# Kernel tuning notes

Measured on AMD Instinct MI355X. Metric: run time of the kernel, lower is better.

Reference implementation:

```python
import jax, jax.numpy as jnp
import numpy as np

N_EMBD = 1024
N_HEAD = 16
HEAD_DIM = N_EMBD // N_HEAD


def setup_inputs() -> dict:
    key = jax.random.key(0)
    ks = jax.random.split(key, 9)
    s = 1.0 / np.sqrt(N_EMBD)
    x = jax.random.normal(ks[0], (2, 2048, N_EMBD), dtype=jnp.float32)
    # PyTorch Linear weights stored as (out_features, in_features)
    Wq = jax.random.uniform(ks[1], (N_EMBD, N_EMBD), jnp.float32, -s, s)
    bq = jax.random.uniform(ks[2], (N_EMBD,), jnp.float32, -s, s)
    Wk = jax.random.uniform(ks[3], (N_EMBD, N_EMBD), jnp.float32, -s, s)
    bk = jax.random.uniform(ks[4], (N_EMBD,), jnp.float32, -s, s)
    Wv = jax.random.uniform(ks[5], (N_EMBD, N_EMBD), jnp.float32, -s, s)
    bv = jax.random.uniform(ks[6], (N_EMBD,), jnp.float32, -s, s)
    Wfc = jax.random.uniform(ks[7], (N_EMBD, N_EMBD), jnp.float32, -s, s)
    bfc = jax.random.uniform(ks[8], (N_EMBD,), jnp.float32, -s, s)
    return {"x": x, "Wq": Wq, "bq": bq, "Wk": Wk, "bk": bk,
            "Wv": Wv, "bv": bv, "Wfc": Wfc, "bfc": bfc}


def reference(x, Wq, bq, Wk, bk, Wv, bv, Wfc, bfc):
    B, S, _ = x.shape

    def proj(W, b):
        y = jnp.einsum('bsd,ed->bse', x, W) + b  # Linear: x @ W.T + b
        return y.reshape(B, S, N_HEAD, HEAD_DIM).transpose(0, 2, 1, 3)  # [B,H,S,Dh]

    q = proj(Wq, bq)
    k = proj(Wk, bk)
    v = proj(Wv, bv)
    scores = jnp.einsum('bhqd,bhkd->bhqk', q, k) / jnp.sqrt(jnp.float32(HEAD_DIM))
    weights = jax.nn.softmax(scores, axis=-1)  # [B,H,S,S]
    out = jnp.einsum('bhqk,bhkd->bhqd', weights, v)
    out = out.transpose(0, 2, 1, 3).reshape(B, S, N_EMBD)
    out = jnp.einsum('bsd,ed->bse', out, Wfc) + bfc
    return (out, weights)
```

## Files before the change

### kernel.cpp

```cpp
#include <hip/hip_runtime.h>
#include <hip/hip_bf16.h>
#include <stdint.h>


typedef __attribute__((ext_vector_type(8))) short bf16x8;
typedef __attribute__((ext_vector_type(4))) short bf16x4;
typedef __attribute__((ext_vector_type(4))) float f32x4;

#define MFMA16(a, b, c) __builtin_amdgcn_mfma_f32_16x16x32_bf16(a, b, c, 0, 0, 0)
#define EXP2(x) __builtin_amdgcn_exp2f(x)

__device__ __forceinline__ short f2bf(float x) {
  uint32_t u = __builtin_bit_cast(uint32_t, x);
  u += 0x7FFFu + ((u >> 16) & 1u);
  return (short)(u >> 16);
}

__device__ __forceinline__ uint32_t cvtpk_bf16(float lo, float hi) {
  uint32_t r;
  asm("v_cvt_pk_bf16_f32 %0, %1, %2" : "=v"(r) : "v"(lo), "v"(hi));
  return r;
}

__device__ __forceinline__ void gload16(const void* g, void* l) {
  __builtin_amdgcn_global_load_lds((const __attribute__((address_space(1))) uint32_t*)g,
                                   (__attribute__((address_space(3))) uint32_t*)l, 16, 0, 0);
}

__global__ __launch_bounds__(256) void cvt_k(const float* __restrict__ src,
                                             short* __restrict__ dst, int n4) {
  int i = blockIdx.x * 256 + threadIdx.x;
  if (i < n4) {
    f32x4 v = *(const f32x4*)(src + (size_t)i * 4);
    bf16x4 o;
    o[0] = f2bf(v[0]); o[1] = f2bf(v[1]); o[2] = f2bf(v[2]); o[3] = f2bf(v[3]);
    *(bf16x4*)(dst + (size_t)i * 4) = o;
  }
}

__global__ __launch_bounds__(256) void cvtw_k(
    const float* __restrict__ w0, const float* __restrict__ w1,
    const float* __restrict__ w2, const float* __restrict__ w3,
    short* __restrict__ dst) {
  const int which = blockIdx.x >> 10;
  const float* src = which == 0 ? w0 : which == 1 ? w1 : which == 2 ? w2 : w3;
  const int i = (blockIdx.x & 1023) * 256 + threadIdx.x;
  f32x4 v = *(const f32x4*)(src + (size_t)i * 4);
  bf16x4 o;
  o[0] = f2bf(v[0]); o[1] = f2bf(v[1]); o[2] = f2bf(v[2]); o[3] = f2bf(v[3]);
  *(bf16x4*)(dst + (size_t)which * 1048576 + (size_t)i * 4) = o;
}

template <int EPI>
__global__ __launch_bounds__(256) void gemm_k(
    const short* __restrict__ A, const short* __restrict__ B,
    const float* __restrict__ bq, const float* __restrict__ bk,
    const float* __restrict__ bv,
    short* __restrict__ Qb, short* __restrict__ Kb, short* __restrict__ Vt,
    float* __restrict__ Fout) {
  const int K = 1024;
  __shared__ short sA[128 * 32];
  __shared__ short sB[128 * 32];
  const int tid = threadIdx.x;
  const int w = tid >> 6, lane = tid & 63;
  const int wr = w >> 1, wc = w & 1;
  const int lrow = lane & 15, lk = (lane >> 4) * 8;
  const int tileM = blockIdx.x * 128, tileN = blockIdx.y * 128;

  f32x4 acc[4][4];
#pragma unroll
  for (int i = 0; i < 4; ++i)
#pragma unroll
    for (int j = 0; j < 4; ++j) acc[i][j] = (f32x4){0.f, 0.f, 0.f, 0.f};

  for (int k0 = 0; k0 < K; k0 += 32) {
#pragma unroll
    for (int i = 0; i < 2; ++i) {
      int u = (w * 2 + i) * 64 + lane;
      int row = u >> 2, c8 = (u & 3) * 8;
      gload16(A + (size_t)(tileM + row) * K + k0 + c8, (short*)sA + (w * 2 + i) * 512);
      gload16(B + (size_t)(tileN + row) * K + k0 + c8, (short*)sB + (w * 2 + i) * 512);
    }
    __syncthreads();
    bf16x8 af[4], bfr[4];
#pragma unroll
    for (int mi = 0; mi < 4; ++mi)
      af[mi] = *(const bf16x8*)&sA[(wr * 64 + mi * 16 + lrow) * 32 + lk];
#pragma unroll
    for (int ni = 0; ni < 4; ++ni)
      bfr[ni] = *(const bf16x8*)&sB[(wc * 64 + ni * 16 + lrow) * 32 + lk];
#pragma unroll
    for (int mi = 0; mi < 4; ++mi)
#pragma unroll
      for (int ni = 0; ni < 4; ++ni)
        acc[mi][ni] = MFMA16(af[mi], bfr[ni], acc[mi][ni]);
    __syncthreads();
  }

#pragma unroll
  for (int mi = 0; mi < 4; ++mi) {
    int m0 = tileM + wr * 64 + mi * 16 + (lane >> 4) * 4;
#pragma unroll
    for (int ni = 0; ni < 4; ++ni) {
      int n = tileN + wc * 64 + ni * 16 + lrow;
      f32x4 v = acc[mi][ni];
      if (EPI == 0) {
        int which = n >> 10, e = n & 1023;
        int h = e >> 6, dh = e & 63;
        float bias = (which == 0 ? bq : which == 1 ? bk : bv)[e];
        int b = m0 >> 11, s0 = m0 & 2047;
        size_t hb = (size_t)(b * 16 + h);
        if (which == 2) {
          int kt2 = s0 >> 5, gl = (s0 >> 3) & 3, ni2 = dh >> 4, j = dh & 15;
          size_t base = (((hb * 64 + kt2) * 4 + ni2) * 64 + gl * 16 + j) * 8 + (s0 & 7);
          bf16x4 pk;
#pragma unroll
          for (int r = 0; r < 4; ++r) pk[r] = f2bf(v[r] + bias);
          *(bf16x4*)&Vt[base] = pk;
        } else {
          short* dst = (which == 0) ? Qb : Kb;
          int tile = s0 >> 4, h2 = dh >> 5, gl = (dh >> 3) & 3, ci = dh & 7;
          size_t base = (((hb * 128 + tile) * 2 + h2) * 64 + gl * 16 + (s0 & 15)) * 8 + ci;
#pragma unroll
          for (int r = 0; r < 4; ++r) dst[base + r * 8] = f2bf(v[r] + bias);
        }
      } else {
        float bias = bq[n];
#pragma unroll
        for (int r = 0; r < 4; ++r)
          Fout[(size_t)(m0 + r) * 1024 + n] = v[r] + bias;
      }
    }
  }
}

__device__ __forceinline__ void sw1_phase(bf16x8& pa, bf16x8& pb, int nxt,
    const short* __restrict__ Kf, int l8, const bf16x8& aQ0, const bf16x8& aQ1,
    float kscale, float& ls0, float& ls1, float& ls2, float& ls3) {
  const f32x4 zero = {0.f, 0.f, 0.f, 0.f};
  __builtin_amdgcn_s_setprio(1);
  f32x4 s = MFMA16(pa, aQ0, zero);
  s = MFMA16(pb, aQ1, s);
  __builtin_amdgcn_s_setprio(0);
  pa = *(const bf16x8*)&Kf[nxt * 1024 + l8];
  pb = *(const bf16x8*)&Kf[nxt * 1024 + 512 + l8];
  ls0 += EXP2(s[0] * kscale);
  ls1 += EXP2(s[1] * kscale);
  ls2 += EXP2(s[2] * kscale);
  ls3 += EXP2(s[3] * kscale);
}

__device__ __forceinline__ void sw2_phase(
    bf16x8& k00, bf16x8& k01, bf16x8& k10, bf16x8& k11,
    bf16x8& v0, bf16x8& v1, bf16x8& v2, bf16x8& v3,
    int kt2, int nxt, short* __restrict__ wl,
    const short* __restrict__ Kw, const short* __restrict__ Vw, int l8,
    const bf16x8& aQ0, const bf16x8& aQ1, float rl, float kscale,
    float* __restrict__ Wqp, int lrow, int g,
    f32x4& o0, f32x4& o1, f32x4& o2, f32x4& o3) {
  const f32x4 zero = {0.f, 0.f, 0.f, 0.f};
  __builtin_amdgcn_s_setprio(1);
  f32x4 sa = MFMA16(k00, aQ0, zero);
  sa = MFMA16(k01, aQ1, sa);
  f32x4 sb = MFMA16(k10, aQ0, zero);
  sb = MFMA16(k11, aQ1, sb);
  __builtin_amdgcn_s_setprio(0);
  const short* Ktn = &Kw[nxt * 2048];
  k00 = *(const bf16x8*)&Ktn[l8];
  k01 = *(const bf16x8*)&Ktn[512 + l8];
  k10 = *(const bf16x8*)&Ktn[1024 + l8];
  k11 = *(const bf16x8*)&Ktn[1536 + l8];
  f32x4 ea, eb;
#pragma unroll
  for (int r = 0; r < 4; ++r) ea[r] = EXP2(sa[r] * kscale) * rl;
#pragma unroll
  for (int r = 0; r < 4; ++r) eb[r] = EXP2(sb[r] * kscale) * rl;
  *(f32x4*)&Wqp[kt2 * 32] = ea;
  *(f32x4*)&Wqp[kt2 * 32 + 16] = eb;
  uint2 pa, pb;
  pa.x = cvtpk_bf16(ea[0], ea[1]);
  pa.y = cvtpk_bf16(ea[2], ea[3]);
  pb.x = cvtpk_bf16(eb[0], eb[1]);
  pb.y = cvtpk_bf16(eb[2], eb[3]);
  *(uint2*)&wl[lrow * 40 + g * 4] = pa;
  *(uint2*)&wl[lrow * 40 + 16 + g * 4] = pb;
  const bf16x8 aW = *(const bf16x8*)&wl[lrow * 40 + g * 8];
  __builtin_amdgcn_s_setprio(1);
  o0 = MFMA16(aW, v0, o0);
  o1 = MFMA16(aW, v1, o1);
  o2 = MFMA16(aW, v2, o2);
  o3 = MFMA16(aW, v3, o3);
  __builtin_amdgcn_s_setprio(0);
  const short* Vpn = &Vw[nxt * 2048];
  v0 = *(const bf16x8*)&Vpn[l8];
  v1 = *(const bf16x8*)&Vpn[512 + l8];
  v2 = *(const bf16x8*)&Vpn[1024 + l8];
  v3 = *(const bf16x8*)&Vpn[1536 + l8];
}

__global__ __launch_bounds__(256, 4) void attn_k(
    const short* __restrict__ Qb, const short* __restrict__ Kb,
    const short* __restrict__ Vt, float* __restrict__ Wout,
    short* __restrict__ attn) {
  __shared__ short Wlds[4][2][16 * 40];
  const int i = blockIdx.x;
  const int bh = ((i & 7) << 2) | ((i >> 3) & 3);
  const int qt = i >> 5;
  const int w = threadIdx.x >> 6, lane = threadIdx.x & 63;
  const int lrow = lane & 15, g = lane >> 4;
  const int qb = qt * 4 + w;
  const int l8 = lane * 8;
  const short* Qf = Qb + (size_t)(bh * 128 + qb) * 1024;
  const short* Kf = Kb + (size_t)bh * (128 * 1024);
  const short* Vf = Vt + (size_t)bh * (64 * 2048);
  const float kscale = 0.125f * 1.44269504088896f;
  const f32x4 zero = {0.f, 0.f, 0.f, 0.f};

  const bf16x8 aQ0 = *(const bf16x8*)&Qf[l8];
  const bf16x8 aQ1 = *(const bf16x8*)&Qf[512 + l8];

  float ls0 = 0.f, ls1 = 0.f, ls2 = 0.f, ls3 = 0.f;
  bf16x8 p0a = *(const bf16x8*)&Kf[0 * 1024 + l8];
  bf16x8 p0b = *(const bf16x8*)&Kf[0 * 1024 + 512 + l8];
  bf16x8 p1a = *(const bf16x8*)&Kf[1 * 1024 + l8];
  bf16x8 p1b = *(const bf16x8*)&Kf[1 * 1024 + 512 + l8];
  bf16x8 p2a = *(const bf16x8*)&Kf[2 * 1024 + l8];
  bf16x8 p2b = *(const bf16x8*)&Kf[2 * 1024 + 512 + l8];
  bf16x8 p3a = *(const bf16x8*)&Kf[3 * 1024 + l8];
  bf16x8 p3b = *(const bf16x8*)&Kf[3 * 1024 + 512 + l8];
  for (int kt = 0; kt < 128; kt += 4) {
    sw1_phase(p0a, p0b, (kt + 4) & 127, Kf, l8, aQ0, aQ1, kscale, ls0, ls1, ls2, ls3);
    sw1_phase(p1a, p1b, (kt + 5) & 127, Kf, l8, aQ0, aQ1, kscale, ls0, ls1, ls2, ls3);
    sw1_phase(p2a, p2b, (kt + 6) & 127, Kf, l8, aQ0, aQ1, kscale, ls0, ls1, ls2, ls3);
    sw1_phase(p3a, p3b, (kt + 7) & 127, Kf, l8, aQ0, aQ1, kscale, ls0, ls1, ls2, ls3);
  }
  float lsum = (ls0 + ls1) + (ls2 + ls3);
  lsum += __shfl_xor(lsum, 16);
  lsum += __shfl_xor(lsum, 32);
  const float rl = 1.0f / lsum;

  f32x4 o0 = zero, o1 = zero, o2 = zero, o3 = zero;
  float* Wqp = Wout + ((size_t)bh * 2048 + qb * 16 + lrow) * 2048 + g * 4;
  short* wlA = &Wlds[w][0][0];
  short* wlB = &Wlds[w][1][0];
  bf16x8 ka00 = *(const bf16x8*)&Kf[l8],        ka01 = *(const bf16x8*)&Kf[512 + l8];
  bf16x8 ka10 = *(const bf16x8*)&Kf[1024 + l8], ka11 = *(const bf16x8*)&Kf[1536 + l8];
  bf16x8 va0 = *(const bf16x8*)&Vf[l8],         va1 = *(const bf16x8*)&Vf[512 + l8];
  bf16x8 va2 = *(const bf16x8*)&Vf[1024 + l8],  va3 = *(const bf16x8*)&Vf[1536 + l8];
  bf16x8 kb00 = *(const bf16x8*)&Kf[2048 + l8], kb01 = *(const bf16x8*)&Kf[2560 + l8];
  bf16x8 kb10 = *(const bf16x8*)&Kf[3072 + l8], kb11 = *(const bf16x8*)&Kf[3584 + l8];
  bf16x8 vb0 = *(const bf16x8*)&Vf[2048 + l8],  vb1 = *(const bf16x8*)&Vf[2560 + l8];
  bf16x8 vb2 = *(const bf16x8*)&Vf[3072 + l8],  vb3 = *(const bf16x8*)&Vf[3584 + l8];
  for (int kt2 = 0; kt2 < 64; kt2 += 2) {
    sw2_phase(ka00, ka01, ka10, ka11, va0, va1, va2, va3,
              kt2, (kt2 + 2) & 63, wlA, Kf, Vf, l8, aQ0, aQ1, rl, kscale,
              Wqp, lrow, g, o0, o1, o2, o3);
    sw2_phase(kb00, kb01, kb10, kb11, vb0, vb1, vb2, vb3,
              kt2 + 1, (kt2 + 3) & 63, wlB, Kf, Vf, l8, aQ0, aQ1, rl, kscale,
              Wqp, lrow, g, o0, o1, o2, o3);
  }

  const int b = bh >> 4, h = bh & 15;
  const size_t obase = (size_t)(b * 2048 + qb * 16 + g * 4) * 1024 + h * 64 + lrow;
#pragma unroll
  for (int r = 0; r < 4; ++r) {
    attn[obase + (size_t)r * 1024 +  0] = f2bf(o0[r]);
    attn[obase + (size_t)r * 1024 + 16] = f2bf(o1[r]);
    attn[obase + (size_t)r * 1024 + 32] = f2bf(o2[r]);
    attn[obase + (size_t)r * 1024 + 48] = f2bf(o3[r]);
  }
}

extern "C" void kernel_launch(void* const* d_in, const int* in_sizes, int n_in,
                              void* d_out, int out_size, void* d_ws,
                              size_t ws_size, hipStream_t stream) {
  const float* x   = (const float*)d_in[0];
  const float* Wq  = (const float*)d_in[1];
  const float* bq  = (const float*)d_in[2];
  const float* Wk  = (const float*)d_in[3];
  const float* bk  = (const float*)d_in[4];
  const float* Wv  = (const float*)d_in[5];
  const float* bv  = (const float*)d_in[6];
  const float* Wfc = (const float*)d_in[7];
  const float* bfc = (const float*)d_in[8];

  float* out  = (float*)d_out;
  float* wout = out + (size_t)4194304;

  char* ws = (char*)d_ws;
  short* xb   = (short*)(ws);
  short* wqkv = (short*)(ws + ((size_t)8  << 20));
  short* wfcb = (short*)(ws + ((size_t)14 << 20));
  short* Qb   = (short*)(ws + ((size_t)16 << 20));
  short* Kb   = (short*)(ws + ((size_t)24 << 20));
  short* Vt   = (short*)(ws + ((size_t)32 << 20));
  short* attn = xb;

  cvt_k<<<4096, 256, 0, stream>>>(x, xb, 1048576);
  cvtw_k<<<4096, 256, 0, stream>>>(Wq, Wk, Wv, Wfc, wqkv);

  gemm_k<0><<<dim3(32, 24), 256, 0, stream>>>(xb, wqkv, bq, bk, bv, Qb, Kb, Vt,
                                              (float*)nullptr);

  attn_k<<<dim3(1024), 256, 0, stream>>>(Qb, Kb, Vt, wout, attn);

  gemm_k<1><<<dim3(32, 8), 256, 0, stream>>>(attn, wfcb, bfc, nullptr, nullptr,
                                             nullptr, nullptr, nullptr, out);
}
```

Measured before the change: 275.9 us.

## Split softmax row-sum pass into separate LDS-staged kernel over key halves

Moves the first attention pass (softmax denominator) out of attn_k into a new kernel that stages K tiles in shared memory, processes two query tiles per wave, and splits the keys into two halves written as partial sums. attn_k then reads the two partial sums instead of recomputing them. This aims to cut redundant global K reads and raise MFMA reuse in the denominator pass. It also drops the setprio hints in the second pass. The cost is an extra kernel launch and a small global round trip for the row sums.

```diff
diff --git a/kernel.cpp b/kernel.cpp
--- a/kernel.cpp
+++ b/kernel.cpp
@@ -134,20 +134,61 @@
   }
 }
 
-__device__ __forceinline__ void sw1_phase(bf16x8& pa, bf16x8& pb, int nxt,
-    const short* __restrict__ Kf, int l8, const bf16x8& aQ0, const bf16x8& aQ1,
-    float kscale, float& ls0, float& ls1, float& ls2, float& ls3) {
+__global__ __launch_bounds__(256) void s1_k(
+    const short* __restrict__ Qb, const short* __restrict__ Kb,
+    float* __restrict__ rsum) {
+  __shared__ __align__(16) short stg[8192];
+  const int i = blockIdx.x;
+  const int bh = ((i & 7) << 2) | ((i >> 3) & 3);
+  const int half = (i >> 5) & 1;
+  const int qc = i >> 6;
+  const int w = threadIdx.x >> 6, lane = threadIdx.x & 63;
+  const int lrow = lane & 15;
+  const int l8 = lane * 8;
+  const int tA = qc * 8 + w * 2;
+  const short* Qf = Qb + (size_t)(bh * 128 + tA) * 1024;
+  const short* KfH = Kb + (size_t)bh * 131072 + (size_t)half * 65536;
+  const float kscale = 0.125f * 1.44269504088896f;
   const f32x4 zero = {0.f, 0.f, 0.f, 0.f};
-  __builtin_amdgcn_s_setprio(1);
-  f32x4 s = MFMA16(pa, aQ0, zero);
-  s = MFMA16(pb, aQ1, s);
-  __builtin_amdgcn_s_setprio(0);
-  pa = *(const bf16x8*)&Kf[nxt * 1024 + l8];
-  pb = *(const bf16x8*)&Kf[nxt * 1024 + 512 + l8];
-  ls0 += EXP2(s[0] * kscale);
-  ls1 += EXP2(s[1] * kscale);
-  ls2 += EXP2(s[2] * kscale);
-  ls3 += EXP2(s[3] * kscale);
+
+  const bf16x8 aQ00 = *(const bf16x8*)&Qf[l8];
+  const bf16x8 aQ01 = *(const bf16x8*)&Qf[512 + l8];
+  const bf16x8 aQ10 = *(const bf16x8*)&Qf[1024 + l8];
+  const bf16x8 aQ11 = *(const bf16x8*)&Qf[1536 + l8];
+
+  float lsA0 = 0.f, lsA1 = 0.f, lsA2 = 0.f, lsA3 = 0.f;
+  float lsB0 = 0.f, lsB1 = 0.f, lsB2 = 0.f, lsB3 = 0.f;
+  for (int b = 0; b < 8; ++b) {
+#pragma unroll
+    for (int p = 0; p < 4; ++p)
+      gload16(KfH + (size_t)b * 8192 + (p * 256 + w * 64 + lane) * 8,
+              (char*)stg + (p * 256 + w * 64) * 16);
+    __syncthreads();
+#pragma unroll
+    for (int t = 0; t < 8; ++t) {
+      bf16x8 k0 = *(const bf16x8*)&stg[t * 1024 + l8];
+      bf16x8 k1 = *(const bf16x8*)&stg[t * 1024 + 512 + l8];
+      f32x4 sA = MFMA16(k0, aQ00, zero); sA = MFMA16(k1, aQ01, sA);
+      f32x4 sB = MFMA16(k0, aQ10, zero); sB = MFMA16(k1, aQ11, sB);
+      lsA0 += EXP2(sA[0] * kscale); lsA1 += EXP2(sA[1] * kscale);
+      lsA2 += EXP2(sA[2] * kscale); lsA3 += EXP2(sA[3] * kscale);
+      lsB0 += EXP2(sB[0] * kscale); lsB1 += EXP2(sB[1] * kscale);
+      lsB2 += EXP2(sB[2] * kscale); lsB3 += EXP2(sB[3] * kscale);
+    }
+    __syncthreads();
+  }
+  float lsumA = (lsA0 + lsA1) + (lsA2 + lsA3);
+  float lsumB = (lsB0 + lsB1) + (lsB2 + lsB3);
+  lsumA += __shfl_xor(lsumA, 16);
+  lsumA += __shfl_xor(lsumA, 32);
+  lsumB += __shfl_xor(lsumB, 16);
+  lsumB += __shfl_xor(lsumB, 32);
+  if (lane < 16) {
+    float* rp = rsum + (size_t)half * 65536 + (size_t)bh * 2048 +
+                qc * 128 + w * 32 + lrow;
+    rp[0] = lsumA;
+    rp[16] = lsumB;
+  }
 }
 
 __device__ __forceinline__ void sw2_phase(
@@ -159,12 +200,10 @@
     float* __restrict__ Wqp, int lrow, int g,
     f32x4& o0, f32x4& o1, f32x4& o2, f32x4& o3) {
   const f32x4 zero = {0.f, 0.f, 0.f, 0.f};
-  __builtin_amdgcn_s_setprio(1);
   f32x4 sa = MFMA16(k00, aQ0, zero);
   sa = MFMA16(k01, aQ1, sa);
   f32x4 sb = MFMA16(k10, aQ0, zero);
   sb = MFMA16(k11, aQ1, sb);
-  __builtin_amdgcn_s_setprio(0);
   const short* Ktn = &Kw[nxt * 2048];
   k00 = *(const bf16x8*)&Ktn[l8];
   k01 = *(const bf16x8*)&Ktn[512 + l8];
@@ -185,12 +224,10 @@
   *(uint2*)&wl[lrow * 40 + g * 4] = pa;
   *(uint2*)&wl[lrow * 40 + 16 + g * 4] = pb;
   const bf16x8 aW = *(const bf16x8*)&wl[lrow * 40 + g * 8];
-  __builtin_amdgcn_s_setprio(1);
   o0 = MFMA16(aW, v0, o0);
   o1 = MFMA16(aW, v1, o1);
   o2 = MFMA16(aW, v2, o2);
   o3 = MFMA16(aW, v3, o3);
-  __builtin_amdgcn_s_setprio(0);
   const short* Vpn = &Vw[nxt * 2048];
   v0 = *(const bf16x8*)&Vpn[l8];
   v1 = *(const bf16x8*)&Vpn[512 + l8];
@@ -200,8 +237,8 @@
 
 __global__ __launch_bounds__(256, 4) void attn_k(
     const short* __restrict__ Qb, const short* __restrict__ Kb,
-    const short* __restrict__ Vt, float* __restrict__ Wout,
-    short* __restrict__ attn) {
+    const short* __restrict__ Vt, const float* __restrict__ rsum,
+    float* __restrict__ Wout, short* __restrict__ attn) {
   __shared__ short Wlds[4][2][16 * 40];
   const int i = blockIdx.x;
   const int bh = ((i & 7) << 2) | ((i >> 3) & 3);
@@ -219,25 +256,8 @@
   const bf16x8 aQ0 = *(const bf16x8*)&Qf[l8];
   const bf16x8 aQ1 = *(const bf16x8*)&Qf[512 + l8];
 
-  float ls0 = 0.f, ls1 = 0.f, ls2 = 0.f, ls3 = 0.f;
-  bf16x8 p0a = *(const bf16x8*)&Kf[0 * 1024 + l8];
-  bf16x8 p0b = *(const bf16x8*)&Kf[0 * 1024 + 512 + l8];
-  bf16x8 p1a = *(const bf16x8*)&Kf[1 * 1024 + l8];
-  bf16x8 p1b = *(const bf16x8*)&Kf[1 * 1024 + 512 + l8];
-  bf16x8 p2a = *(const bf16x8*)&Kf[2 * 1024 + l8];
-  bf16x8 p2b = *(const bf16x8*)&Kf[2 * 1024 + 512 + l8];
-  bf16x8 p3a = *(const bf16x8*)&Kf[3 * 1024 + l8];
-  bf16x8 p3b = *(const bf16x8*)&Kf[3 * 1024 + 512 + l8];
-  for (int kt = 0; kt < 128; kt += 4) {
-    sw1_phase(p0a, p0b, (kt + 4) & 127, Kf, l8, aQ0, aQ1, kscale, ls0, ls1, ls2, ls3);
-    sw1_phase(p1a, p1b, (kt + 5) & 127, Kf, l8, aQ0, aQ1, kscale, ls0, ls1, ls2, ls3);
-    sw1_phase(p2a, p2b, (kt + 6) & 127, Kf, l8, aQ0, aQ1, kscale, ls0, ls1, ls2, ls3);
-    sw1_phase(p3a, p3b, (kt + 7) & 127, Kf, l8, aQ0, aQ1, kscale, ls0, ls1, ls2, ls3);
-  }
-  float lsum = (ls0 + ls1) + (ls2 + ls3);
-  lsum += __shfl_xor(lsum, 16);
-  lsum += __shfl_xor(lsum, 32);
-  const float rl = 1.0f / lsum;
+  const size_t ri = (size_t)bh * 2048 + qb * 16 + lrow;
+  const float rl = 1.0f / (rsum[ri] + rsum[65536 + ri]);
 
   f32x4 o0 = zero, o1 = zero, o2 = zero, o3 = zero;
   float* Wqp = Wout + ((size_t)bh * 2048 + qb * 16 + lrow) * 2048 + g * 4;
@@ -294,6 +314,7 @@
   short* Qb   = (short*)(ws + ((size_t)16 << 20));
   short* Kb   = (short*)(ws + ((size_t)24 << 20));
   short* Vt   = (short*)(ws + ((size_t)32 << 20));
+  float* rsum = (float*)(ws + ((size_t)40 << 20));
   short* attn = xb;
 
   cvt_k<<<4096, 256, 0, stream>>>(x, xb, 1048576);
@@ -302,7 +323,9 @@
   gemm_k<0><<<dim3(32, 24), 256, 0, stream>>>(xb, wqkv, bq, bk, bv, Qb, Kb, Vt,
                                               (float*)nullptr);
 
-  attn_k<<<dim3(1024), 256, 0, stream>>>(Qb, Kb, Vt, wout, attn);
+  s1_k<<<dim3(1024), 256, 0, stream>>>(Qb, Kb, rsum);
+
+  attn_k<<<dim3(1024), 256, 0, stream>>>(Qb, Kb, Vt, rsum, wout, attn);
 
   gemm_k<1><<<dim3(32, 8), 256, 0, stream>>>(attn, wfcb, bfc, nullptr, nullptr,
                                              nullptr, nullptr, nullptr, out);
```

Result: no change. 279.5 us (+1.3%).

## Stage softmax weight tiles in LDS for coalesced row stores; drop setprio

Applied to the files above, without the earlier changes.

Softmax probabilities are now written into a per-wave padded LDS buffer and then copied out as 64-float contiguous row segments. Previously each lane stored scattered 16-byte pieces directly to global memory. The change targets better write coalescing for the large weights output, at the cost of extra LDS traffic and a larger LDS footprint. It also removes the s_setprio hints around the MFMA groups.

```diff
diff --git a/kernel.cpp b/kernel.cpp
--- a/kernel.cpp
+++ b/kernel.cpp
@@ -138,10 +138,8 @@
     const short* __restrict__ Kf, int l8, const bf16x8& aQ0, const bf16x8& aQ1,
     float kscale, float& ls0, float& ls1, float& ls2, float& ls3) {
   const f32x4 zero = {0.f, 0.f, 0.f, 0.f};
-  __builtin_amdgcn_s_setprio(1);
   f32x4 s = MFMA16(pa, aQ0, zero);
   s = MFMA16(pb, aQ1, s);
-  __builtin_amdgcn_s_setprio(0);
   pa = *(const bf16x8*)&Kf[nxt * 1024 + l8];
   pb = *(const bf16x8*)&Kf[nxt * 1024 + 512 + l8];
   ls0 += EXP2(s[0] * kscale);
@@ -153,18 +151,16 @@
 __device__ __forceinline__ void sw2_phase(
     bf16x8& k00, bf16x8& k01, bf16x8& k10, bf16x8& k11,
     bf16x8& v0, bf16x8& v1, bf16x8& v2, bf16x8& v3,
-    int kt2, int nxt, short* __restrict__ wl,
+    int nxt, short* __restrict__ wl, float* __restrict__ wb,
     const short* __restrict__ Kw, const short* __restrict__ Vw, int l8,
     const bf16x8& aQ0, const bf16x8& aQ1, float rl, float kscale,
-    float* __restrict__ Wqp, int lrow, int g,
+    int lrow, int g,
     f32x4& o0, f32x4& o1, f32x4& o2, f32x4& o3) {
   const f32x4 zero = {0.f, 0.f, 0.f, 0.f};
-  __builtin_amdgcn_s_setprio(1);
   f32x4 sa = MFMA16(k00, aQ0, zero);
   sa = MFMA16(k01, aQ1, sa);
   f32x4 sb = MFMA16(k10, aQ0, zero);
   sb = MFMA16(k11, aQ1, sb);
-  __builtin_amdgcn_s_setprio(0);
   const short* Ktn = &Kw[nxt * 2048];
   k00 = *(const bf16x8*)&Ktn[l8];
   k01 = *(const bf16x8*)&Ktn[512 + l8];
@@ -175,8 +171,8 @@
   for (int r = 0; r < 4; ++r) ea[r] = EXP2(sa[r] * kscale) * rl;
 #pragma unroll
   for (int r = 0; r < 4; ++r) eb[r] = EXP2(sb[r] * kscale) * rl;
-  *(f32x4*)&Wqp[kt2 * 32] = ea;
-  *(f32x4*)&Wqp[kt2 * 32 + 16] = eb;
+  *(f32x4*)&wb[lrow * 68 + g * 4] = ea;
+  *(f32x4*)&wb[lrow * 68 + 16 + g * 4] = eb;
   uint2 pa, pb;
   pa.x = cvtpk_bf16(ea[0], ea[1]);
   pa.y = cvtpk_bf16(ea[2], ea[3]);
@@ -185,12 +181,10 @@
   *(uint2*)&wl[lrow * 40 + g * 4] = pa;
   *(uint2*)&wl[lrow * 40 + 16 + g * 4] = pb;
   const bf16x8 aW = *(const bf16x8*)&wl[lrow * 40 + g * 8];
-  __builtin_amdgcn_s_setprio(1);
   o0 = MFMA16(aW, v0, o0);
   o1 = MFMA16(aW, v1, o1);
   o2 = MFMA16(aW, v2, o2);
   o3 = MFMA16(aW, v3, o3);
-  __builtin_amdgcn_s_setprio(0);
   const short* Vpn = &Vw[nxt * 2048];
   v0 = *(const bf16x8*)&Vpn[l8];
   v1 = *(const bf16x8*)&Vpn[512 + l8];
@@ -203,6 +197,7 @@
     const short* __restrict__ Vt, float* __restrict__ Wout,
     short* __restrict__ attn) {
   __shared__ short Wlds[4][2][16 * 40];
+  __shared__ float Wbuf[4][16 * 68];
   const int i = blockIdx.x;
   const int bh = ((i & 7) << 2) | ((i >> 3) & 3);
   const int qt = i >> 5;
@@ -240,9 +235,10 @@
   const float rl = 1.0f / lsum;
 
   f32x4 o0 = zero, o1 = zero, o2 = zero, o3 = zero;
-  float* Wqp = Wout + ((size_t)bh * 2048 + qb * 16 + lrow) * 2048 + g * 4;
+  float* Wrow = Wout + ((size_t)bh * 2048 + qb * 16) * 2048;
   short* wlA = &Wlds[w][0][0];
   short* wlB = &Wlds[w][1][0];
+  float* wb0 = &Wbuf[w][0];
   bf16x8 ka00 = *(const bf16x8*)&Kf[l8],        ka01 = *(const bf16x8*)&Kf[512 + l8];
   bf16x8 ka10 = *(const bf16x8*)&Kf[1024 + l8], ka11 = *(const bf16x8*)&Kf[1536 + l8];
   bf16x8 va0 = *(const bf16x8*)&Vf[l8],         va1 = *(const bf16x8*)&Vf[512 + l8];
@@ -253,11 +249,22 @@
   bf16x8 vb2 = *(const bf16x8*)&Vf[3072 + l8],  vb3 = *(const bf16x8*)&Vf[3584 + l8];
   for (int kt2 = 0; kt2 < 64; kt2 += 2) {
     sw2_phase(ka00, ka01, ka10, ka11, va0, va1, va2, va3,
-              kt2, (kt2 + 2) & 63, wlA, Kf, Vf, l8, aQ0, aQ1, rl, kscale,
-              Wqp, lrow, g, o0, o1, o2, o3);
+              (kt2 + 2) & 63, wlA, wb0, Kf, Vf, l8, aQ0, aQ1, rl, kscale,
+              lrow, g, o0, o1, o2, o3);
     sw2_phase(kb00, kb01, kb10, kb11, vb0, vb1, vb2, vb3,
-              kt2 + 1, (kt2 + 3) & 63, wlB, Kf, Vf, l8, aQ0, aQ1, rl, kscale,
-              Wqp, lrow, g, o0, o1, o2, o3);
+              (kt2 + 3) & 63, wlB, wb0 + 32, Kf, Vf, l8, aQ0, aQ1, rl, kscale,
+              lrow, g, o0, o1, o2, o3);
+    {
+      const int kb = kt2 >> 1;
+      const int fr = lane >> 4;
+      const int fc = (lane & 15) * 4;
+#pragma unroll
+      for (int j = 0; j < 4; ++j) {
+        const int row = j * 4 + fr;
+        f32x4 t = *(const f32x4*)&wb0[row * 68 + fc];
+        *(f32x4*)&Wrow[(size_t)row * 2048 + kb * 64 + fc] = t;
+      }
+    }
   }
 
   const int b = bh >> 4, h = bh & 15;
```

Result: no change. 280.9 us (+1.8%).
